# Kernel tuning notes

Hardware: AMD Instinct MI355X
Metric: run time of the kernel (lower is better)

Reference implementation:

```python
import math
import jax, jax.numpy as jnp
import numpy as np

HIDDEN = 256
HEADS = 8
HEAD_DIM = HIDDEN // HEADS


def setup_inputs() -> dict:
    key = jax.random.key(0)
    ks = jax.random.split(key, 8)
    b, n = 2, 4096
    node_state = jax.random.normal(ks[0], (b, n, HIDDEN), dtype=jnp.float32)
    adjacency = jax.random.uniform(ks[1], (b, n, n), dtype=jnp.float32)
    s = 1.0 / math.sqrt(HIDDEN)
    Wq = jax.random.uniform(ks[2], (HIDDEN, HIDDEN), jnp.float32, -s, s)
    Wk = jax.random.uniform(ks[3], (HIDDEN, HIDDEN), jnp.float32, -s, s)
    Wv = jax.random.uniform(ks[4], (HIDDEN, HIDDEN), jnp.float32, -s, s)
    Wo = jax.random.uniform(ks[5], (HIDDEN, HIDDEN), jnp.float32, -s, s)
    bo = jax.random.uniform(ks[6], (HIDDEN,), jnp.float32, -s, s)
    return {"node_state": node_state, "adjacency": adjacency,
            "Wq": Wq, "Wk": Wk, "Wv": Wv, "Wo": Wo, "bo": bo}


def reference(node_state, adjacency, Wq, Wk, Wv, Wo, bo):
    b, n, _ = node_state.shape
    # torch Linear: x @ W.T ; reshape to (b, h, n, d)
    def split_heads(x):
        return x.reshape(b, n, HEADS, HEAD_DIM).transpose(0, 2, 1, 3)
    q = split_heads(node_state @ Wq.T)
    k = split_heads(node_state @ Wk.T)
    v = split_heads(node_state @ Wv.T)
    scores = jnp.einsum('bhqd,bhkd->bhqk', q, k) / math.sqrt(HEAD_DIM)
    log_adj = jnp.log(adjacency + 1e-6)           # (b, n, n)
    scores = scores + log_adj[:, None, :, :]       # broadcast over heads
    attn = jax.nn.softmax(scores, axis=-1)         # dropout=0.0 -> identity
    out = jnp.einsum('bhqk,bhkd->bhqd', attn, v)
    out = out.transpose(0, 2, 1, 3).reshape(b, n, HIDDEN)
    return out @ Wo.T + bo
```

## Files before the change

kernel.cpp:

```cpp
#include <hip/hip_runtime.h>
#include <hip/hip_bf16.h>

typedef __attribute__((ext_vector_type(8))) __bf16 bf16x8;
typedef __attribute__((ext_vector_type(4))) float f32x4;
typedef __attribute__((ext_vector_type(8))) unsigned short u16x8;
typedef __attribute__((ext_vector_type(4))) unsigned short u16x4;

__device__ __forceinline__ unsigned short f2bf(float f) {
  unsigned u = __builtin_bit_cast(unsigned, f);
  u += 0x7FFFu + ((u >> 16) & 1u);
  return (unsigned short)(u >> 16);
}

__device__ __forceinline__ bf16x8 ldb8(const unsigned short* p) {
  return *reinterpret_cast<const bf16x8*>(p);
}

__device__ __forceinline__ bf16x8 cvt8v(const float4 a, const float4 b) {
  u16x8 r;
  r[0] = f2bf(a.x); r[1] = f2bf(a.y); r[2] = f2bf(a.z); r[3] = f2bf(a.w);
  r[4] = f2bf(b.x); r[5] = f2bf(b.y); r[6] = f2bf(b.z); r[7] = f2bf(b.w);
  return __builtin_bit_cast(bf16x8, r);
}

__global__ __launch_bounds__(256) void wconv(
    const float* __restrict__ Wq, const float* __restrict__ Wk,
    const float* __restrict__ Wv, const float* __restrict__ Wo,
    unsigned short* __restrict__ Wb) {
  int i = blockIdx.x * 256 + threadIdx.x;
  const float s = 0.17677669529663687f;
  Wb[i]          = f2bf(Wq[i] * s);
  Wb[65536 + i]  = f2bf(Wk[i]);
  Wb[131072 + i] = f2bf(Wv[i]);
  Wb[196608 + i] = f2bf(Wo[i]);
}

__global__ __launch_bounds__(256) void qkv_proj(
    const float* __restrict__ X, const unsigned short* __restrict__ Wb,
    unsigned short* __restrict__ Qb, unsigned short* __restrict__ Kb,
    unsigned short* __restrict__ Vt) {
  int bid = blockIdx.x;
  int m = bid >> 8;
  int r0 = (bid & 255) * 32;
  int tid = threadIdx.x, lane = tid & 63, wave = tid >> 6;
  int wr = (wave >> 1) * 16, wc = (wave & 1) * 128;
  int lr = lane & 15, kgrp = (lane >> 4) * 8;
  const unsigned short* W = Wb + m * 65536;
  int arow = r0 + wr + lr;

  bf16x8 afrag[8];
#pragma unroll
  for (int k = 0; k < 8; ++k) {
    const float* p = &X[arow * 256 + k * 32 + kgrp];
    float4 a = *reinterpret_cast<const float4*>(p);
    float4 b = *reinterpret_cast<const float4*>(p + 4);
    afrag[k] = cvt8v(a, b);
  }

#pragma unroll
  for (int t = 0; t < 8; ++t) {
    int c0 = wc + t * 16;
    int wrow = c0 + lr;
    f32x4 acc = {0.f, 0.f, 0.f, 0.f};
#pragma unroll
    for (int k = 0; k < 8; ++k) {
      bf16x8 bfrag = ldb8(&W[wrow * 256 + k * 32 + kgrp]);
      acc = __builtin_amdgcn_mfma_f32_16x16x32_bf16(afrag[k], bfrag, acc, 0, 0, 0);
    }
    int col = c0 + lr;
    int h = col >> 5, d = col & 31;
#pragma unroll
    for (int e = 0; e < 4; ++e) {
      int gr = r0 + wr + (lane >> 4) * 4 + e;
      int b = gr >> 12, nq = gr & 4095;
      unsigned short v = f2bf(acc[e]);
      if (m == 0)      Qb[((b * 8 + h) * 4096 + nq) * 32 + d] = v;
      else if (m == 1) Kb[((b * 8 + h) * 4096 + nq) * 32 + d] = v;
      else             Vt[((b * 8 + h) * 32 + d) * 4096 + nq] = v;
    }
  }
}

__global__ __launch_bounds__(256, 3) void attn(
    const unsigned short* __restrict__ Qb, const unsigned short* __restrict__ Kb,
    const unsigned short* __restrict__ Vt, const float* __restrict__ Adj,
    float* __restrict__ Opart, float* __restrict__ Ml) {
  int rid = blockIdx.x;
  int cid = (rid & 7) * 256 + (rid >> 3);
  int hg = cid & 1;
  int qb = (cid >> 1) & 127;
  int c  = cid >> 8;
  int b = c >> 2, ks = c & 3;
  int q0 = qb * 32;
  int k_base = ks * 1024;

  int tid = threadIdx.x, lane = tid & 63, w = tid >> 6;
  int h = hg * 4 + w;
  int lr = lane & 15, lg = lane >> 4;

  __shared__ unsigned short plds[4][32][72];

  const unsigned short* Qh = Qb + (size_t)(b * 8 + h) * 4096 * 32;
  const unsigned short* Kh = Kb + (size_t)(b * 8 + h) * 4096 * 32;
  const unsigned short* Vh = Vt + (size_t)(b * 8 + h) * 32 * 4096;
  const float* adjB = Adj + (size_t)b * 4096 * 4096;

  const f32x4 Z4 = {0.f, 0.f, 0.f, 0.f};
  const float LOG2E = 1.4426950408889634f;

  bf16x8 qfrag[2];
#pragma unroll
  for (int qt = 0; qt < 2; ++qt)
    qfrag[qt] = ldb8(&Qh[(q0 + qt * 16 + lr) * 32 + lg * 8]);

  size_t arow[2][4];
#pragma unroll
  for (int qt = 0; qt < 2; ++qt)
#pragma unroll
    for (int r = 0; r < 4; ++r)
      arow[qt][r] = (size_t)(q0 + qt * 16 + lg * 4 + r) * 4096;

  float mrow[2][4], lrow[2][4];
  f32x4 oacc[2][2];
#pragma unroll
  for (int qt = 0; qt < 2; ++qt) {
#pragma unroll
    for (int r = 0; r < 4; ++r) { mrow[qt][r] = -1e30f; lrow[qt][r] = 0.f; }
    oacc[qt][0] = Z4; oacc[qt][1] = Z4;
  }

  for (int kt0 = k_base; kt0 < k_base + 1024; kt0 += 64) {
    f32x4 sacc[2][4];
#pragma unroll
    for (int kt = 0; kt < 4; ++kt) {
      bf16x8 kf = ldb8(&Kh[(kt0 + kt * 16 + lr) * 32 + lg * 8]);
#pragma unroll
      for (int qt = 0; qt < 2; ++qt)
        sacc[qt][kt] = __builtin_amdgcn_mfma_f32_16x16x32_bf16(qfrag[qt], kf, Z4, 0, 0, 0);
    }

    float adjv[2][4][4];
#pragma unroll
    for (int qt = 0; qt < 2; ++qt)
#pragma unroll
      for (int kt = 0; kt < 4; ++kt)
#pragma unroll
        for (int r = 0; r < 4; ++r)
          adjv[qt][kt][r] = adjB[arow[qt][r] + kt0 + kt * 16 + lr];

    float mnew[2][4], mm[2][4], sc[2][4];
#pragma unroll
    for (int qt = 0; qt < 2; ++qt)
#pragma unroll
      for (int r = 0; r < 4; ++r) {
        float v = fmaxf(fmaxf(sacc[qt][0][r], sacc[qt][1][r]),
                        fmaxf(sacc[qt][2][r], sacc[qt][3][r]));
#pragma unroll
        for (int off = 8; off >= 1; off >>= 1)
          v = fmaxf(v, __shfl_xor(v, off));
        mnew[qt][r] = fmaxf(mrow[qt][r], v);
        sc[qt][r] = __builtin_amdgcn_exp2f((mrow[qt][r] - mnew[qt][r]) * LOG2E);
        mrow[qt][r] = mnew[qt][r];
        lrow[qt][r] *= sc[qt][r];
        mm[qt][r] = mnew[qt][r] * LOG2E;
      }
#pragma unroll
    for (int qt = 0; qt < 2; ++qt)
#pragma unroll
      for (int dt = 0; dt < 2; ++dt)
#pragma unroll
        for (int r = 0; r < 4; ++r)
          oacc[qt][dt][r] *= sc[qt][r];

    float rs[2][4] = {};
#pragma unroll
    for (int qt = 0; qt < 2; ++qt)
#pragma unroll
      for (int kt = 0; kt < 4; ++kt)
#pragma unroll
        for (int r = 0; r < 4; ++r) {
          int row = qt * 16 + lg * 4 + r;
          float e = __builtin_amdgcn_exp2f(
              __builtin_fmaf(sacc[qt][kt][r], LOG2E, -mm[qt][r]));
          float p = (adjv[qt][kt][r] + 1e-6f) * e;
          rs[qt][r] += p;
          unsigned u = __builtin_bit_cast(unsigned, p) + 0x8000u;
          plds[w][row][kt * 16 + lr] = (unsigned short)(u >> 16);
        }
#pragma unroll
    for (int qt = 0; qt < 2; ++qt)
#pragma unroll
      for (int r = 0; r < 4; ++r) {
        float v = rs[qt][r];
#pragma unroll
        for (int off = 8; off >= 1; off >>= 1)
          v += __shfl_xor(v, off);
        lrow[qt][r] += v;
      }

    asm volatile("s_waitcnt lgkmcnt(0)" ::: "memory");

#pragma unroll
    for (int kc = 0; kc < 2; ++kc) {
      bf16x8 vf[2];
#pragma unroll
      for (int dt = 0; dt < 2; ++dt)
        vf[dt] = ldb8(&Vh[(dt * 16 + lr) * 4096 + kt0 + kc * 32 + lg * 8]);
      bf16x8 pf[2];
#pragma unroll
      for (int qt = 0; qt < 2; ++qt)
        pf[qt] = ldb8(&plds[w][qt * 16 + lr][kc * 32 + lg * 8]);
#pragma unroll
      for (int qt = 0; qt < 2; ++qt)
#pragma unroll
        for (int dt = 0; dt < 2; ++dt)
          oacc[qt][dt] = __builtin_amdgcn_mfma_f32_16x16x32_bf16(pf[qt], vf[dt], oacc[qt][dt], 0, 0, 0);
    }
  }

  float* Op = Opart + ((((size_t)ks * 2 + b) * 128 + qb) * 8 + h) * 1024;
#pragma unroll
  for (int qt = 0; qt < 2; ++qt)
#pragma unroll
    for (int r = 0; r < 4; ++r) {
      int row = qt * 16 + lg * 4 + r;
#pragma unroll
      for (int dt = 0; dt < 2; ++dt)
        Op[row * 32 + dt * 16 + lr] = oacc[qt][dt][r];
    }
  float* MlP = Ml + ((((size_t)ks * 2 + b) * 128 + qb) * 8 + h) * 64;
  if (lr == 0) {
#pragma unroll
    for (int qt = 0; qt < 2; ++qt)
#pragma unroll
      for (int r = 0; r < 4; ++r) {
        int row = qt * 16 + lg * 4 + r;
        MlP[row * 2]     = mrow[qt][r];
        MlP[row * 2 + 1] = lrow[qt][r];
      }
  }
}

__global__ __launch_bounds__(256) void combine(
    const float* __restrict__ Opart, const float* __restrict__ Ml,
    unsigned short* __restrict__ AObf) {
  int bid = blockIdx.x;
  int b = bid >> 10, qb = (bid >> 3) & 127, h = bid & 7;
  int tid = threadIdx.x, row = tid >> 3, cg = (tid & 7) * 4;
  size_t base = (((size_t)b * 128 + qb) * 8 + h);
  const size_t ostr = 2097152, mstr = 131072;

  float m[4], l[4];
#pragma unroll
  for (int s = 0; s < 4; ++s) {
    const float* p = Ml + s * mstr + base * 64 + row * 2;
    m[s] = p[0]; l[s] = p[1];
  }
  float M = fmaxf(fmaxf(m[0], m[1]), fmaxf(m[2], m[3]));
  float e[4], L = 0.f;
#pragma unroll
  for (int s = 0; s < 4; ++s) { e[s] = __expf(m[s] - M); L += l[s] * e[s]; }
  float invL = 1.0f / L;

  float4 acc = {0.f, 0.f, 0.f, 0.f};
#pragma unroll
  for (int s = 0; s < 4; ++s) {
    float4 o = *reinterpret_cast<const float4*>(
        Opart + s * ostr + base * 1024 + row * 32 + cg);
    acc.x += o.x * e[s]; acc.y += o.y * e[s];
    acc.z += o.z * e[s]; acc.w += o.w * e[s];
  }
  u16x4 r4;
  r4[0] = f2bf(acc.x * invL); r4[1] = f2bf(acc.y * invL);
  r4[2] = f2bf(acc.z * invL); r4[3] = f2bf(acc.w * invL);
  size_t orow = ((size_t)b * 4096 + qb * 32 + row) * 256 + h * 32 + cg;
  *reinterpret_cast<u16x4*>(AObf + orow) = r4;
}

__global__ __launch_bounds__(256) void out_proj(
    const unsigned short* __restrict__ AObf, const unsigned short* __restrict__ Wob,
    const float* __restrict__ bo, float* __restrict__ Out) {
  int r0 = blockIdx.x * 32;
  int tid = threadIdx.x, lane = tid & 63, wave = tid >> 6;
  int wr = (wave >> 1) * 16, wc = (wave & 1) * 128;
  int lr = lane & 15, kgrp = (lane >> 4) * 8;
  int arow = r0 + wr + lr;

  bf16x8 afrag[8];
#pragma unroll
  for (int k = 0; k < 8; ++k)
    afrag[k] = ldb8(&AObf[arow * 256 + k * 32 + kgrp]);

#pragma unroll
  for (int t = 0; t < 8; ++t) {
    int c0 = wc + t * 16;
    int wrow = c0 + lr;
    f32x4 acc = {0.f, 0.f, 0.f, 0.f};
#pragma unroll
    for (int k = 0; k < 8; ++k) {
      bf16x8 bfrag = ldb8(&Wob[wrow * 256 + k * 32 + kgrp]);
      acc = __builtin_amdgcn_mfma_f32_16x16x32_bf16(afrag[k], bfrag, acc, 0, 0, 0);
    }
    float bias = bo[c0 + lr];
#pragma unroll
    for (int e = 0; e < 4; ++e) {
      int gr = r0 + wr + (lane >> 4) * 4 + e;
      Out[(size_t)gr * 256 + c0 + lr] = acc[e] + bias;
    }
  }
}

extern "C" void kernel_launch(void* const* d_in, const int* in_sizes, int n_in,
                              void* d_out, int out_size, void* d_ws, size_t ws_size,
                              hipStream_t stream) {
  const float* X   = (const float*)d_in[0];
  const float* Adj = (const float*)d_in[1];
  const float* Wq  = (const float*)d_in[2];
  const float* Wk  = (const float*)d_in[3];
  const float* Wv  = (const float*)d_in[4];
  const float* Wo  = (const float*)d_in[5];
  const float* bo  = (const float*)d_in[6];
  float* Out = (float*)d_out;

  unsigned short* ws = (unsigned short*)d_ws;
  unsigned short* Wb   = ws;
  unsigned short* Qb   = ws + 262144;
  unsigned short* Kb   = Qb + 2097152;
  unsigned short* Vt   = Kb + 2097152;
  unsigned short* AObf = Vt + 2097152;
  float* Opart = (float*)(AObf + 2097152);
  float* Ml    = Opart + 4 * 2097152;

  hipLaunchKernelGGL(wconv,    dim3(256),  dim3(256), 0, stream, Wq, Wk, Wv, Wo, Wb);
  hipLaunchKernelGGL(qkv_proj, dim3(768),  dim3(256), 0, stream, X, Wb, Qb, Kb, Vt);
  hipLaunchKernelGGL(attn,     dim3(2048), dim3(256), 0, stream, Qb, Kb, Vt, Adj, Opart, Ml);
  hipLaunchKernelGGL(combine,  dim3(2048), dim3(256), 0, stream, Opart, Ml, AObf);
  hipLaunchKernelGGL(out_proj, dim3(256),  dim3(256), 0, stream, AObf, Wb + 196608, bo, Out);
}
```

Measured before the change: 201.8 us.

## Transpose QK MFMA so P stays in registers, dropping LDS round-trip

Swaps the operand order of the QK^T MFMA so each lane holds four consecutive keys of one query row. The probabilities can then be packed straight into bf16 registers with v_cvt_pk_bf16_f32 and fed to a 16x16x16 MFMA against V. This removes the shared-memory staging buffer and its wait, and replaces the 4-step row-max and row-sum shuffle reductions with 2 steps. Adjacency loads and output stores become float4 vectors, and the occupancy hint rises from 3 to 4 blocks. The risks are the narrower-K MFMA issuing more instructions and possible register pressure under the tighter launch bound.

```diff
diff --git a/kernel.cpp b/kernel.cpp
--- a/kernel.cpp
+++ b/kernel.cpp
@@ -5,6 +5,8 @@
 typedef __attribute__((ext_vector_type(4))) float f32x4;
 typedef __attribute__((ext_vector_type(8))) unsigned short u16x8;
 typedef __attribute__((ext_vector_type(4))) unsigned short u16x4;
+typedef __attribute__((ext_vector_type(4))) short s16x4;
+typedef __attribute__((ext_vector_type(2))) unsigned u32x2;
 
 __device__ __forceinline__ unsigned short f2bf(float f) {
   unsigned u = __builtin_bit_cast(unsigned, f);
@@ -21,6 +23,19 @@
   r[0] = f2bf(a.x); r[1] = f2bf(a.y); r[2] = f2bf(a.z); r[3] = f2bf(a.w);
   r[4] = f2bf(b.x); r[5] = f2bf(b.y); r[6] = f2bf(b.z); r[7] = f2bf(b.w);
   return __builtin_bit_cast(bf16x8, r);
+}
+
+__device__ __forceinline__ unsigned cvtpk(float a, float b) {
+  unsigned r;
+  asm("v_cvt_pk_bf16_f32 %0, %1, %2" : "=v"(r) : "v"(a), "v"(b));
+  return r;
+}
+
+__device__ __forceinline__ f32x4 max4(f32x4 a, f32x4 b) {
+  f32x4 r;
+  r[0] = fmaxf(a[0], b[0]); r[1] = fmaxf(a[1], b[1]);
+  r[2] = fmaxf(a[2], b[2]); r[3] = fmaxf(a[3], b[3]);
+  return r;
 }
 
 __global__ __launch_bounds__(256) void wconv(
@@ -81,7 +96,7 @@
   }
 }
 
-__global__ __launch_bounds__(256, 3) void attn(
+__global__ __launch_bounds__(256, 4) void attn(
     const unsigned short* __restrict__ Qb, const unsigned short* __restrict__ Kb,
     const unsigned short* __restrict__ Vt, const float* __restrict__ Adj,
     float* __restrict__ Opart, float* __restrict__ Ml) {
@@ -97,8 +112,7 @@
   int tid = threadIdx.x, lane = tid & 63, w = tid >> 6;
   int h = hg * 4 + w;
   int lr = lane & 15, lg = lane >> 4;
-
-  __shared__ unsigned short plds[4][32][72];
+  int lg4 = lg * 4;
 
   const unsigned short* Qh = Qb + (size_t)(b * 8 + h) * 4096 * 32;
   const unsigned short* Kh = Kb + (size_t)(b * 8 + h) * 4096 * 32;
@@ -113,108 +127,86 @@
   for (int qt = 0; qt < 2; ++qt)
     qfrag[qt] = ldb8(&Qh[(q0 + qt * 16 + lr) * 32 + lg * 8]);
 
-  size_t arow[2][4];
+  size_t arow[2];
 #pragma unroll
   for (int qt = 0; qt < 2; ++qt)
-#pragma unroll
-    for (int r = 0; r < 4; ++r)
-      arow[qt][r] = (size_t)(q0 + qt * 16 + lg * 4 + r) * 4096;
-
-  float mrow[2][4], lrow[2][4];
+    arow[qt] = (size_t)(q0 + qt * 16 + lr) * 4096;
+
+  float mrow[2] = {-1e30f, -1e30f}, lrow[2] = {0.f, 0.f};
   f32x4 oacc[2][2];
-#pragma unroll
-  for (int qt = 0; qt < 2; ++qt) {
-#pragma unroll
-    for (int r = 0; r < 4; ++r) { mrow[qt][r] = -1e30f; lrow[qt][r] = 0.f; }
-    oacc[qt][0] = Z4; oacc[qt][1] = Z4;
-  }
+  oacc[0][0] = Z4; oacc[0][1] = Z4; oacc[1][0] = Z4; oacc[1][1] = Z4;
 
   for (int kt0 = k_base; kt0 < k_base + 1024; kt0 += 64) {
     f32x4 sacc[2][4];
 #pragma unroll
     for (int kt = 0; kt < 4; ++kt) {
       bf16x8 kf = ldb8(&Kh[(kt0 + kt * 16 + lr) * 32 + lg * 8]);
-#pragma unroll
-      for (int qt = 0; qt < 2; ++qt)
-        sacc[qt][kt] = __builtin_amdgcn_mfma_f32_16x16x32_bf16(qfrag[qt], kf, Z4, 0, 0, 0);
-    }
-
-    float adjv[2][4][4];
+      sacc[0][kt] = __builtin_amdgcn_mfma_f32_16x16x32_bf16(kf, qfrag[0], Z4, 0, 0, 0);
+      sacc[1][kt] = __builtin_amdgcn_mfma_f32_16x16x32_bf16(kf, qfrag[1], Z4, 0, 0, 0);
+    }
+
+    float4 ad[2][4];
 #pragma unroll
     for (int qt = 0; qt < 2; ++qt)
 #pragma unroll
       for (int kt = 0; kt < 4; ++kt)
-#pragma unroll
-        for (int r = 0; r < 4; ++r)
-          adjv[qt][kt][r] = adjB[arow[qt][r] + kt0 + kt * 16 + lr];
-
-    float mnew[2][4], mm[2][4], sc[2][4];
-#pragma unroll
-    for (int qt = 0; qt < 2; ++qt)
-#pragma unroll
-      for (int r = 0; r < 4; ++r) {
-        float v = fmaxf(fmaxf(sacc[qt][0][r], sacc[qt][1][r]),
-                        fmaxf(sacc[qt][2][r], sacc[qt][3][r]));
-#pragma unroll
-        for (int off = 8; off >= 1; off >>= 1)
-          v = fmaxf(v, __shfl_xor(v, off));
-        mnew[qt][r] = fmaxf(mrow[qt][r], v);
-        sc[qt][r] = __builtin_amdgcn_exp2f((mrow[qt][r] - mnew[qt][r]) * LOG2E);
-        mrow[qt][r] = mnew[qt][r];
-        lrow[qt][r] *= sc[qt][r];
-        mm[qt][r] = mnew[qt][r] * LOG2E;
+        ad[qt][kt] = *reinterpret_cast<const float4*>(
+            &adjB[arow[qt] + kt0 + kt * 16 + lg4]);
+
+    float mm[2], sc[2];
+#pragma unroll
+    for (int qt = 0; qt < 2; ++qt) {
+      f32x4 t = max4(max4(sacc[qt][0], sacc[qt][1]),
+                     max4(sacc[qt][2], sacc[qt][3]));
+      float v = fmaxf(fmaxf(t[0], t[1]), fmaxf(t[2], t[3]));
+      v = fmaxf(v, __shfl_xor(v, 16));
+      v = fmaxf(v, __shfl_xor(v, 32));
+      float mnew = fmaxf(mrow[qt], v);
+      sc[qt] = __builtin_amdgcn_exp2f((mrow[qt] - mnew) * LOG2E);
+      mrow[qt] = mnew;
+      lrow[qt] *= sc[qt];
+      mm[qt] = mnew * LOG2E;
+#pragma unroll
+      for (int dt = 0; dt < 2; ++dt)
+#pragma unroll
+        for (int e = 0; e < 4; ++e)
+          oacc[qt][dt][e] *= sc[qt];
+    }
+
+    f32x4 rsv[2] = {Z4, Z4};
+#pragma unroll
+    for (int kt = 0; kt < 4; ++kt) {
+      s16x4 vf[2];
+#pragma unroll
+      for (int dt = 0; dt < 2; ++dt)
+        vf[dt] = *reinterpret_cast<const s16x4*>(
+            &Vh[(dt * 16 + lr) * 4096 + kt0 + kt * 16 + lg4]);
+#pragma unroll
+      for (int qt = 0; qt < 2; ++qt) {
+        float p0 = (ad[qt][kt].x + 1e-6f) *
+            __builtin_amdgcn_exp2f(__builtin_fmaf(sacc[qt][kt][0], LOG2E, -mm[qt]));
+        float p1 = (ad[qt][kt].y + 1e-6f) *
+            __builtin_amdgcn_exp2f(__builtin_fmaf(sacc[qt][kt][1], LOG2E, -mm[qt]));
+        float p2 = (ad[qt][kt].z + 1e-6f) *
+            __builtin_amdgcn_exp2f(__builtin_fmaf(sacc[qt][kt][2], LOG2E, -mm[qt]));
+        float p3 = (ad[qt][kt].w + 1e-6f) *
+            __builtin_amdgcn_exp2f(__builtin_fmaf(sacc[qt][kt][3], LOG2E, -mm[qt]));
+        rsv[qt][0] += p0; rsv[qt][1] += p1; rsv[qt][2] += p2; rsv[qt][3] += p3;
+        unsigned w0 = cvtpk(p0, p1), w1 = cvtpk(p2, p3);
+        s16x4 pb = __builtin_bit_cast(s16x4, (u32x2){w0, w1});
+#pragma unroll
+        for (int dt = 0; dt < 2; ++dt)
+          oacc[qt][dt] = __builtin_amdgcn_mfma_f32_16x16x16bf16_1k(
+              vf[dt], pb, oacc[qt][dt], 0, 0, 0);
       }
-#pragma unroll
-    for (int qt = 0; qt < 2; ++qt)
-#pragma unroll
-      for (int dt = 0; dt < 2; ++dt)
-#pragma unroll
-        for (int r = 0; r < 4; ++r)
-          oacc[qt][dt][r] *= sc[qt][r];
-
-    float rs[2][4] = {};
-#pragma unroll
-    for (int qt = 0; qt < 2; ++qt)
-#pragma unroll
-      for (int kt = 0; kt < 4; ++kt)
-#pragma unroll
-        for (int r = 0; r < 4; ++r) {
-          int row = qt * 16 + lg * 4 + r;
-          float e = __builtin_amdgcn_exp2f(
-              __builtin_fmaf(sacc[qt][kt][r], LOG2E, -mm[qt][r]));
-          float p = (adjv[qt][kt][r] + 1e-6f) * e;
-          rs[qt][r] += p;
-          unsigned u = __builtin_bit_cast(unsigned, p) + 0x8000u;
-          plds[w][row][kt * 16 + lr] = (unsigned short)(u >> 16);
-        }
-#pragma unroll
-    for (int qt = 0; qt < 2; ++qt)
-#pragma unroll
-      for (int r = 0; r < 4; ++r) {
-        float v = rs[qt][r];
-#pragma unroll
-        for (int off = 8; off >= 1; off >>= 1)
-          v += __shfl_xor(v, off);
-        lrow[qt][r] += v;
-      }
-
-    asm volatile("s_waitcnt lgkmcnt(0)" ::: "memory");
-
-#pragma unroll
-    for (int kc = 0; kc < 2; ++kc) {
-      bf16x8 vf[2];
-#pragma unroll
-      for (int dt = 0; dt < 2; ++dt)
-        vf[dt] = ldb8(&Vh[(dt * 16 + lr) * 4096 + kt0 + kc * 32 + lg * 8]);
-      bf16x8 pf[2];
-#pragma unroll
-      for (int qt = 0; qt < 2; ++qt)
-        pf[qt] = ldb8(&plds[w][qt * 16 + lr][kc * 32 + lg * 8]);
-#pragma unroll
-      for (int qt = 0; qt < 2; ++qt)
-#pragma unroll
-        for (int dt = 0; dt < 2; ++dt)
-          oacc[qt][dt] = __builtin_amdgcn_mfma_f32_16x16x32_bf16(pf[qt], vf[dt], oacc[qt][dt], 0, 0, 0);
+    }
+
+#pragma unroll
+    for (int qt = 0; qt < 2; ++qt) {
+      float rs = (rsv[qt][0] + rsv[qt][1]) + (rsv[qt][2] + rsv[qt][3]);
+      rs += __shfl_xor(rs, 16);
+      rs += __shfl_xor(rs, 32);
+      lrow[qt] += rs;
     }
   }
 
@@ -222,22 +214,16 @@
 #pragma unroll
   for (int qt = 0; qt < 2; ++qt)
 #pragma unroll
-    for (int r = 0; r < 4; ++r) {
-      int row = qt * 16 + lg * 4 + r;
-#pragma unroll
-      for (int dt = 0; dt < 2; ++dt)
-        Op[row * 32 + dt * 16 + lr] = oacc[qt][dt][r];
-    }
+    for (int dt = 0; dt < 2; ++dt)
+      *reinterpret_cast<f32x4*>(&Op[(qt * 16 + lr) * 32 + dt * 16 + lg4]) =
+          oacc[qt][dt];
   float* MlP = Ml + ((((size_t)ks * 2 + b) * 128 + qb) * 8 + h) * 64;
-  if (lr == 0) {
-#pragma unroll
-    for (int qt = 0; qt < 2; ++qt)
-#pragma unroll
-      for (int r = 0; r < 4; ++r) {
-        int row = qt * 16 + lg * 4 + r;
-        MlP[row * 2]     = mrow[qt][r];
-        MlP[row * 2 + 1] = lrow[qt][r];
-      }
+  if (lane < 16) {
+#pragma unroll
+    for (int qt = 0; qt < 2; ++qt) {
+      float2 ml = {mrow[qt], lrow[qt]};
+      *reinterpret_cast<float2*>(&MlP[(qt * 16 + lr) * 2]) = ml;
+    }
   }
 }
 
```

Result: slower. 314.7 us (+56.0%).
